# Optimization experiments

Measured on AMD Instinct MI355X. Metric: run time of the kernel, lower is better.

## Reference

```python
import jax, jax.numpy as jnp
import numpy as np

N_NODES = 100_000
N_EDGES = 800_000
N_GRAPHS = 2048
D = 64
NUM_REL = 5
PROP_STEPS = 6
S2S_STEPS = 6


def setup_inputs() -> dict:
    key = jax.random.key(0)
    ks = jax.random.split(key, 16)
    x = jax.random.normal(ks[0], (N_NODES, 15), jnp.float32)
    edge_index = jax.random.randint(ks[1], (2, N_EDGES), 0, N_NODES)
    edge_type = jax.random.randint(ks[2], (N_EDGES,), 0, NUM_REL)
    batch = jnp.sort(jax.random.randint(ks[3], (N_NODES,), 0, N_GRAPHS))

    def lin(k, i, o):
        return jax.random.normal(k, (i, o), jnp.float32) / np.sqrt(i).astype(np.float32)

    return {
        'x': x, 'edge_index': edge_index, 'edge_type': edge_type, 'batch': batch,
        'lin0_w': lin(ks[4], 15, D), 'lin0_b': jnp.zeros((D,), jnp.float32),
        'basis': jax.random.normal(ks[5], (NUM_REL, D, D), jnp.float32) / np.sqrt(D).astype(np.float32),
        'att': jax.random.normal(ks[6], (NUM_REL, NUM_REL), jnp.float32) / np.sqrt(NUM_REL).astype(np.float32),
        'root': lin(ks[7], D, D), 'conv_b': jnp.zeros((D,), jnp.float32),
        'w_ih': jax.random.normal(ks[8], (4 * D, 2 * D), jnp.float32) / np.sqrt(2 * D).astype(np.float32),
        'w_hh': jax.random.normal(ks[9], (4 * D, D), jnp.float32) / np.sqrt(D).astype(np.float32),
        'b_ih': jnp.zeros((4 * D,), jnp.float32), 'b_hh': jnp.zeros((4 * D,), jnp.float32),
        'lin1_w': lin(ks[10], 2 * D, D), 'lin1_b': jnp.zeros((D,), jnp.float32),
        'lin2_w': lin(ks[11], D, 12), 'lin2_b': jnp.zeros((12,), jnp.float32),
    }


def _rgcn_conv(h, src, dst, edge_type, W, root, bias):
    # W: [R, D, D]; transform all nodes per relation, then gather per edge.
    n = h.shape[0]
    h_rel = jnp.einsum('nd,rde->rne', h, W)            # [R, N, D]
    msg = h_rel[edge_type, src]                        # [E, D] gather
    agg = jnp.zeros_like(h).at[dst].add(msg)           # scatter-add
    cnt = jnp.zeros((n,), h.dtype).at[dst].add(1.0)
    agg = agg / jnp.maximum(cnt, 1.0)[:, None]         # mean aggregation
    return agg + h @ root + bias


def _set2set(h, batch, w_ih, w_hh, b_ih, b_hh):
    d = h.shape[1]
    q_star = jnp.zeros((N_GRAPHS, 2 * d), h.dtype)
    hx = jnp.zeros((N_GRAPHS, d), h.dtype)
    cx = jnp.zeros((N_GRAPHS, d), h.dtype)
    for _ in range(S2S_STEPS):
        gates = q_star @ w_ih.T + b_ih + hx @ w_hh.T + b_hh
        i, f, g, o = jnp.split(gates, 4, axis=-1)
        cx = jax.nn.sigmoid(f) * cx + jax.nn.sigmoid(i) * jnp.tanh(g)
        hx = jax.nn.sigmoid(o) * jnp.tanh(cx)
        q = hx                                          # [B, D]
        e = jnp.sum(h * q[batch], axis=-1)              # [N]
        m = jax.ops.segment_max(e, batch, num_segments=N_GRAPHS)
        a = jnp.exp(e - m[batch])
        s = jax.ops.segment_sum(a, batch, num_segments=N_GRAPHS)
        a = a / s[batch]                                # segment softmax
        r = jax.ops.segment_sum(a[:, None] * h, batch, num_segments=N_GRAPHS)
        q_star = jnp.concatenate([q, r], axis=-1)
    return q_star


def reference(x, edge_index, edge_type, batch, lin0_w, lin0_b, basis, att, root,
              conv_b, w_ih, w_hh, b_ih, b_hh, lin1_w, lin1_b, lin2_w, lin2_b):
    W = jnp.einsum('rb,bde->rde', att, basis)           # basis decomposition
    h = jax.nn.relu(x @ lin0_w + lin0_b)
    src, dst = edge_index[0], edge_index[1]
    for _ in range(PROP_STEPS):
        h = jax.nn.relu(_rgcn_conv(h, src, dst, edge_type, W, root, conv_b))
    q = _set2set(h, batch, w_ih, w_hh, b_ih, b_hh)      # [B, 2D]
    out = jax.nn.relu(q @ lin1_w + lin1_b)
    return out @ lin2_w + lin2_b                        # [B, 12]
```

## Files before the change

### kernel.cpp

```cpp
#include <hip/hip_runtime.h>
#include <hip/hip_bf16.h>
#include <math.h>

#define NN 100000
#define NE 800000
#define NG 2048
#define DD 64
#define NR 5
#define KK 384
#define NB ((NN + 255) / 256)
#define CAP 96

typedef __attribute__((ext_vector_type(8))) short bf16x8;
typedef __attribute__((ext_vector_type(4))) float f32x4;
typedef unsigned short ushort_t;
typedef unsigned int uint_t;

static __device__ __forceinline__ float sigmoidf_(float x) { return 1.0f / (1.0f + expf(-x)); }

static __device__ __forceinline__ ushort_t f2bf(float f) {
    uint_t u = __float_as_uint(f);
    uint_t r = (u + 0x7FFFu + ((u >> 16) & 1u)) >> 16;
    return (ushort_t)r;
}
static __device__ __forceinline__ float bf2f(ushort_t b) {
    return __uint_as_float(((uint_t)b) << 16);
}

__global__ void k_w2(const float* __restrict__ att, const float* __restrict__ basis,
                     const float* __restrict__ root, ushort_t* __restrict__ wt_hi,
                     ushort_t* __restrict__ wt_lo) {
    int i = blockIdx.x * blockDim.x + threadIdx.x;
    if (i >= DD * KK) return;
    int c = i / KK;
    int k = i % KK;
    int t = k >> 6;
    int kd = k & 63;
    float w;
    if (t < NR) {
        w = 0.f;
#pragma unroll
        for (int b = 0; b < NR; ++b) w += att[t * NR + b] * basis[(b * DD + kd) * DD + c];
    } else {
        w = root[kd * DD + c];
    }
    ushort_t hi = f2bf(w);
    ushort_t lo = f2bf(w - bf2f(hi));
    wt_hi[c * KK + k] = hi;
    wt_lo[c * KK + k] = lo;
}

__global__ void k_wf(const float* __restrict__ wih, const float* __restrict__ whh,
                     const float* __restrict__ bih, const float* __restrict__ bhh,
                     float* __restrict__ Wq, float* __restrict__ Wr, float* __restrict__ Wb) {
    int i = blockIdx.x * blockDim.x + threadIdx.x;
    if (i >= 256 * 64) return;
    int j = i >> 6, c = i & 63;
    Wq[i] = wih[j * 128 + c] + whh[i];
    Wr[i] = wih[j * 128 + 64 + c];
    if (c == 0) Wb[j] = bih[j] + bhh[j];
}

__global__ void k_cnt(const int* __restrict__ dst, int* __restrict__ deg) {
    int e = blockIdx.x * blockDim.x + threadIdx.x;
    if (e < NE) atomicAdd(&deg[dst[e]], 1);
}

__global__ void k_scan1(const int* __restrict__ deg, int* __restrict__ part,
                        int* __restrict__ bsum) {
    __shared__ int s[256];
    int tid = threadIdx.x;
    int i = blockIdx.x * 256 + tid;
    int v = (i < NN) ? deg[i] : 0;
    s[tid] = v;
    __syncthreads();
    for (int off = 1; off < 256; off <<= 1) {
        int t = (tid >= off) ? s[tid - off] : 0;
        __syncthreads();
        s[tid] += t;
        __syncthreads();
    }
    if (i < NN) part[i] = s[tid] - v;
    if (tid == 255) bsum[blockIdx.x] = s[255];
}

__global__ void k_scan2(int* __restrict__ bsum) {
    __shared__ int s[512];
    int tid = threadIdx.x;
    int v = (tid < NB) ? bsum[tid] : 0;
    s[tid] = v;
    __syncthreads();
    for (int off = 1; off < 512; off <<= 1) {
        int t = (tid >= off) ? s[tid - off] : 0;
        __syncthreads();
        s[tid] += t;
        __syncthreads();
    }
    if (tid < NB) bsum[tid] = s[tid] - v;
}

__global__ void k_scan3(const int* __restrict__ part, const int* __restrict__ bsum,
                        const int* __restrict__ deg, int* __restrict__ rowptr,
                        float* __restrict__ invc) {
    int i = blockIdx.x * blockDim.x + threadIdx.x;
    if (i >= NN) return;
    rowptr[i] = part[i] + bsum[i >> 8];
    invc[i] = 1.0f / fmaxf((float)deg[i], 1.0f);
    if (i == 0) rowptr[NN] = NE;
}

__global__ void k_fill(const int* __restrict__ src, const int* __restrict__ dst,
                       const int* __restrict__ et, int* __restrict__ cur,
                       int* __restrict__ eidx) {
    int e = blockIdx.x * blockDim.x + threadIdx.x;
    if (e >= NE) return;
    int d = dst[e];
    int pos = atomicAdd(&cur[d], 1);
    eidx[pos] = src[e] | (et[e] << 20);
}

__global__ void k_seg(const int* __restrict__ batch, int* __restrict__ seg) {
    int g = blockIdx.x * blockDim.x + threadIdx.x;
    if (g > NG) return;
    int lo = 0, hi = NN;
    while (lo < hi) {
        int mid = (lo + hi) >> 1;
        if (batch[mid] < g) lo = mid + 1; else hi = mid;
    }
    seg[g] = lo;
}

__global__ void k_lin0(const float* __restrict__ x, const float* __restrict__ w,
                       const float* __restrict__ b, float* __restrict__ h) {
    int lane = threadIdx.x & 63, wave = threadIdx.x >> 6;
    float Wc[15];
#pragma unroll
    for (int k = 0; k < 15; ++k) Wc[k] = w[k * DD + lane];
    float bias = b[lane];
    int n0 = blockIdx.x * 256;
    int n1 = min(n0 + 256, NN);
    for (int n = n0 + wave; n < n1; n += 4) {
        int nu = __builtin_amdgcn_readfirstlane(n);
        const float* xr = x + (size_t)nu * 15;
        float a = bias;
#pragma unroll
        for (int k = 0; k < 15; ++k) a += xr[k] * Wc[k];
        h[(size_t)nu * DD + lane] = fmaxf(a, 0.f);
    }
}

__global__ void __launch_bounds__(512) k_conv(
        const float* __restrict__ h, const int* __restrict__ eidx,
        const int* __restrict__ rowptr, const float* __restrict__ invc,
        const ushort_t* __restrict__ wt_hi, const ushort_t* __restrict__ wt_lo,
        const float* __restrict__ bias, float* __restrict__ hout) {
    __shared__ ushort_t lhi[32][392];
    __shared__ ushort_t llo[32][392];
    int tid = threadIdx.x;
    int lane = tid & 63, w = tid >> 6;
    int n0 = blockIdx.x * 32;

    for (int i = 0; i < 4; ++i) {
        int row = w * 4 + i;
        int n = __builtin_amdgcn_readfirstlane(n0 + row);
        int r0 = rowptr[n], r1 = rowptr[n + 1];
        float a0 = 0.f, a1 = 0.f, a2 = 0.f, a3 = 0.f, a4 = 0.f;
        int e = r0;
        for (; e + 8 <= r1; e += 8) {
            int p0 = eidx[e + 0], p1 = eidx[e + 1], p2 = eidx[e + 2], p3 = eidx[e + 3];
            int p4 = eidx[e + 4], p5 = eidx[e + 5], p6 = eidx[e + 6], p7 = eidx[e + 7];
            float v0 = h[(size_t)(p0 & 0xFFFFF) * DD + lane];
            float v1 = h[(size_t)(p1 & 0xFFFFF) * DD + lane];
            float v2 = h[(size_t)(p2 & 0xFFFFF) * DD + lane];
            float v3 = h[(size_t)(p3 & 0xFFFFF) * DD + lane];
            float v4 = h[(size_t)(p4 & 0xFFFFF) * DD + lane];
            float v5 = h[(size_t)(p5 & 0xFFFFF) * DD + lane];
            float v6 = h[(size_t)(p6 & 0xFFFFF) * DD + lane];
            float v7 = h[(size_t)(p7 & 0xFFFFF) * DD + lane];
            int t0 = p0 >> 20, t1 = p1 >> 20, t2 = p2 >> 20, t3 = p3 >> 20;
            int t4 = p4 >> 20, t5 = p5 >> 20, t6 = p6 >> 20, t7 = p7 >> 20;
            a0 += (t0 == 0 ? v0 : 0.f) + (t1 == 0 ? v1 : 0.f) + (t2 == 0 ? v2 : 0.f) + (t3 == 0 ? v3 : 0.f)
                + (t4 == 0 ? v4 : 0.f) + (t5 == 0 ? v5 : 0.f) + (t6 == 0 ? v6 : 0.f) + (t7 == 0 ? v7 : 0.f);
            a1 += (t0 == 1 ? v0 : 0.f) + (t1 == 1 ? v1 : 0.f) + (t2 == 1 ? v2 : 0.f) + (t3 == 1 ? v3 : 0.f)
                + (t4 == 1 ? v4 : 0.f) + (t5 == 1 ? v5 : 0.f) + (t6 == 1 ? v6 : 0.f) + (t7 == 1 ? v7 : 0.f);
            a2 += (t0 == 2 ? v0 : 0.f) + (t1 == 2 ? v1 : 0.f) + (t2 == 2 ? v2 : 0.f) + (t3 == 2 ? v3 : 0.f)
                + (t4 == 2 ? v4 : 0.f) + (t5 == 2 ? v5 : 0.f) + (t6 == 2 ? v6 : 0.f) + (t7 == 2 ? v7 : 0.f);
            a3 += (t0 == 3 ? v0 : 0.f) + (t1 == 3 ? v1 : 0.f) + (t2 == 3 ? v2 : 0.f) + (t3 == 3 ? v3 : 0.f)
                + (t4 == 3 ? v4 : 0.f) + (t5 == 3 ? v5 : 0.f) + (t6 == 3 ? v6 : 0.f) + (t7 == 3 ? v7 : 0.f);
            a4 += (t0 == 4 ? v0 : 0.f) + (t1 == 4 ? v1 : 0.f) + (t2 == 4 ? v2 : 0.f) + (t3 == 4 ? v3 : 0.f)
                + (t4 == 4 ? v4 : 0.f) + (t5 == 4 ? v5 : 0.f) + (t6 == 4 ? v6 : 0.f) + (t7 == 4 ? v7 : 0.f);
        }
        for (; e + 4 <= r1; e += 4) {
            int p0 = eidx[e + 0], p1 = eidx[e + 1], p2 = eidx[e + 2], p3 = eidx[e + 3];
            float v0 = h[(size_t)(p0 & 0xFFFFF) * DD + lane];
            float v1 = h[(size_t)(p1 & 0xFFFFF) * DD + lane];
            float v2 = h[(size_t)(p2 & 0xFFFFF) * DD + lane];
            float v3 = h[(size_t)(p3 & 0xFFFFF) * DD + lane];
            int t0 = p0 >> 20, t1 = p1 >> 20, t2 = p2 >> 20, t3 = p3 >> 20;
            a0 += (t0 == 0 ? v0 : 0.f) + (t1 == 0 ? v1 : 0.f) + (t2 == 0 ? v2 : 0.f) + (t3 == 0 ? v3 : 0.f);
            a1 += (t0 == 1 ? v0 : 0.f) + (t1 == 1 ? v1 : 0.f) + (t2 == 1 ? v2 : 0.f) + (t3 == 1 ? v3 : 0.f);
            a2 += (t0 == 2 ? v0 : 0.f) + (t1 == 2 ? v1 : 0.f) + (t2 == 2 ? v2 : 0.f) + (t3 == 2 ? v3 : 0.f);
            a3 += (t0 == 3 ? v0 : 0.f) + (t1 == 3 ? v1 : 0.f) + (t2 == 3 ? v2 : 0.f) + (t3 == 3 ? v3 : 0.f);
            a4 += (t0 == 4 ? v0 : 0.f) + (t1 == 4 ? v1 : 0.f) + (t2 == 4 ? v2 : 0.f) + (t3 == 4 ? v3 : 0.f);
        }
        for (; e < r1; ++e) {
            int p = eidx[e];
            float v = h[(size_t)(p & 0xFFFFF) * DD + lane];
            int t = p >> 20;
            a0 += (t == 0) ? v : 0.f;
            a1 += (t == 1) ? v : 0.f;
            a2 += (t == 2) ? v : 0.f;
            a3 += (t == 3) ? v : 0.f;
            a4 += (t == 4) ? v : 0.f;
        }
        float ic = invc[n];
        float vals[6];
        vals[0] = a0 * ic; vals[1] = a1 * ic; vals[2] = a2 * ic;
        vals[3] = a3 * ic; vals[4] = a4 * ic;
        vals[5] = h[(size_t)n * DD + lane];
#pragma unroll
        for (int t = 0; t < 6; ++t) {
            ushort_t hi = f2bf(vals[t]);
            ushort_t lo = f2bf(vals[t] - bf2f(hi));
            lhi[row][t * 64 + lane] = hi;
            llo[row][t * 64 + lane] = lo;
        }
    }
    __syncthreads();

    int rg = w & 1;
    int ct = w >> 1;
    int crow = lane & 15, kb = lane >> 4;
    const ushort_t* pbh = wt_hi + (size_t)(ct * 16 + crow) * KK + kb * 8;
    const ushort_t* pbl = wt_lo + (size_t)(ct * 16 + crow) * KK + kb * 8;
    f32x4 acc = (f32x4){0.f, 0.f, 0.f, 0.f};
#pragma unroll 3
    for (int ks = 0; ks < 12; ++ks) {
        bf16x8 ahi = *(const bf16x8*)&lhi[rg * 16 + crow][ks * 32 + kb * 8];
        bf16x8 alo = *(const bf16x8*)&llo[rg * 16 + crow][ks * 32 + kb * 8];
        bf16x8 bhi = *(const bf16x8*)(pbh + ks * 32);
        bf16x8 blo = *(const bf16x8*)(pbl + ks * 32);
        acc = __builtin_amdgcn_mfma_f32_16x16x32_bf16(ahi, bhi, acc, 0, 0, 0);
        acc = __builtin_amdgcn_mfma_f32_16x16x32_bf16(ahi, blo, acc, 0, 0, 0);
        acc = __builtin_amdgcn_mfma_f32_16x16x32_bf16(alo, bhi, acc, 0, 0, 0);
    }
    float bv = bias[ct * 16 + crow];
#pragma unroll
    for (int r = 0; r < 4; ++r) {
        int n = n0 + rg * 16 + kb * 4 + r;
        hout[(size_t)n * DD + ct * 16 + crow] = fmaxf(acc[r] + bv, 0.f);
    }
}

__global__ void __launch_bounds__(256) k_s2s6(
        const float* __restrict__ h, const int* __restrict__ seg,
        const float* __restrict__ Wq, const float* __restrict__ Wr,
        const float* __restrict__ Wb, float* __restrict__ qstar) {
    int g = blockIdx.x;
    int tid = threadIdx.x;
    int lane = tid & 63, wave = tid >> 6;
    __shared__ float hsm[CAP][65];
    __shared__ float a_s[256];
    __shared__ float gates_s[256];
    __shared__ float hx_s[64], cx_s[64], r_s[64];
    __shared__ float red_s[4][64];
    __shared__ float m_s, sum_s;

    int s0 = seg[g], s1 = seg[g + 1];
    int len = min(s1 - s0, 256);
    int cap = min(len, CAP);
    for (int i = tid; i < cap * 64; i += 256) {
        int row = i >> 6, c = i & 63;
        hsm[row][c] = h[(size_t)(s0 + row) * DD + c];
    }
    if (tid < 64) { hx_s[tid] = 0.f; cx_s[tid] = 0.f; r_s[tid] = 0.f; }
    __syncthreads();

    for (int step = 0; step < 6; ++step) {
        {
            float acc = Wb[tid];
            const float4* wq4 = (const float4*)(Wq + (size_t)tid * DD);
            const float4* wr4 = (const float4*)(Wr + (size_t)tid * DD);
            const float4* hx4 = (const float4*)hx_s;
            const float4* rr4 = (const float4*)r_s;
#pragma unroll 4
            for (int k4 = 0; k4 < 16; ++k4) {
                float4 wv = wq4[k4], hv = hx4[k4];
                acc += wv.x * hv.x + wv.y * hv.y + wv.z * hv.z + wv.w * hv.w;
            }
#pragma unroll 4
            for (int k4 = 0; k4 < 16; ++k4) {
                float4 wv = wr4[k4], rv = rr4[k4];
                acc += wv.x * rv.x + wv.y * rv.y + wv.z * rv.z + wv.w * rv.w;
            }
            gates_s[tid] = acc;
        }
        __syncthreads();
        if (tid < 64) {
            float iv = sigmoidf_(gates_s[tid]);
            float fv = sigmoidf_(gates_s[64 + tid]);
            float gv = tanhf(gates_s[128 + tid]);
            float ov = sigmoidf_(gates_s[192 + tid]);
            float cc = fv * cx_s[tid] + iv * gv;
            cx_s[tid] = cc;
            hx_s[tid] = ov * tanhf(cc);
        }
        __syncthreads();

        for (int row = tid; row < len; row += 256) {
            const float* hr = (row < CAP) ? &hsm[row][0] : &h[(size_t)(s0 + row) * DD];
            float e = 0.f;
#pragma unroll 8
            for (int c = 0; c < 64; ++c) e += hr[c] * hx_s[c];
            a_s[row] = e;
        }
        __syncthreads();
        if (wave == 0) {
            float mm = -INFINITY;
            for (int row = lane; row < len; row += 64) mm = fmaxf(mm, a_s[row]);
#pragma unroll
            for (int off = 32; off >= 1; off >>= 1) mm = fmaxf(mm, __shfl_xor(mm, off, 64));
            if (lane == 0) m_s = mm;
        }
        __syncthreads();
        float m = m_s;
        for (int row = tid; row < len; row += 256) a_s[row] = expf(a_s[row] - m);
        __syncthreads();
        if (wave == 0) {
            float ss = 0.f;
            for (int row = lane; row < len; row += 64) ss += a_s[row];
#pragma unroll
            for (int off = 32; off >= 1; off >>= 1) ss += __shfl_xor(ss, off, 64);
            if (lane == 0) sum_s = ss;
        }
        __syncthreads();
        float racc = 0.f;
        for (int row = wave; row < len; row += 4) {
            const float* hr = (row < CAP) ? &hsm[row][0] : &h[(size_t)(s0 + row) * DD];
            racc += a_s[row] * hr[lane];
        }
        red_s[wave][lane] = racc;
        __syncthreads();
        if (tid < 64) {
            float r = red_s[0][tid] + red_s[1][tid] + red_s[2][tid] + red_s[3][tid];
            float s = sum_s;
            r_s[tid] = (s > 0.f) ? (r / s) : 0.f;
        }
        __syncthreads();
    }
    if (tid < 64) {
        qstar[(size_t)g * 2 * DD + tid] = hx_s[tid];
        qstar[(size_t)g * 2 * DD + DD + tid] = r_s[tid];
    }
}

__global__ void k_final(const float* __restrict__ qstar, const float* __restrict__ w1,
                        const float* __restrict__ b1, const float* __restrict__ w2,
                        const float* __restrict__ b2, float* __restrict__ out) {
    int g = blockIdx.x;
    int j = threadIdx.x;
    float a = b1[j];
    const float* qs = qstar + (size_t)g * 2 * DD;
#pragma unroll 16
    for (int k = 0; k < 2 * DD; ++k) a += qs[k] * w1[k * DD + j];
    float t = fmaxf(a, 0.f);
    __shared__ float ts[64];
    ts[j] = t;
    __syncthreads();
    if (j < 12) {
        float o = b2[j];
#pragma unroll 16
        for (int d = 0; d < DD; ++d) o += ts[d] * w2[d * 12 + j];
        out[(size_t)g * 12 + j] = o;
    }
}

extern "C" void kernel_launch(void* const* d_in, const int* in_sizes, int n_in,
                              void* d_out, int out_size, void* d_ws, size_t ws_size,
                              hipStream_t stream) {
    const float* x     = (const float*)d_in[0];
    const int*   ei    = (const int*)d_in[1];
    const int*   etype = (const int*)d_in[2];
    const int*   batch = (const int*)d_in[3];
    const float* l0w   = (const float*)d_in[4];
    const float* l0b   = (const float*)d_in[5];
    const float* basis = (const float*)d_in[6];
    const float* att   = (const float*)d_in[7];
    const float* root  = (const float*)d_in[8];
    const float* convb = (const float*)d_in[9];
    const float* wih   = (const float*)d_in[10];
    const float* whh   = (const float*)d_in[11];
    const float* bih   = (const float*)d_in[12];
    const float* bhh   = (const float*)d_in[13];
    const float* l1w   = (const float*)d_in[14];
    const float* l1b   = (const float*)d_in[15];
    const float* l2w   = (const float*)d_in[16];
    const float* l2b   = (const float*)d_in[17];
    const int* src = ei;
    const int* dst = ei + NE;
    float* out = (float*)d_out;

    char* ws = (char*)d_ws;
    size_t off = 0;
    auto alloc = [&](size_t bytes) {
        void* p = ws + off;
        off = (off + bytes + 255) & ~(size_t)255;
        return p;
    };
    ushort_t* wt_hi = (ushort_t*)alloc((size_t)DD * KK * 2);
    ushort_t* wt_lo = (ushort_t*)alloc((size_t)DD * KK * 2);
    float* Wq     = (float*)alloc((size_t)256 * 64 * 4);
    float* Wr     = (float*)alloc((size_t)256 * 64 * 4);
    float* Wb     = (float*)alloc((size_t)256 * 4);
    float* h_a    = (float*)alloc((size_t)NN * DD * 4);
    float* h_b    = (float*)alloc((size_t)NN * DD * 4);
    int*   deg    = (int*)alloc((size_t)NN * 4);
    float* invc   = (float*)alloc((size_t)NN * 4);
    int*   part   = (int*)alloc((size_t)NN * 4);
    int*   bsum   = (int*)alloc((size_t)512 * 4);
    int*   rowptr = (int*)alloc((size_t)(NN + 1) * 4);
    int*   cur    = (int*)alloc((size_t)NN * 4);
    int*   eidx   = (int*)alloc((size_t)NE * 4);
    int*   seg    = (int*)alloc((size_t)(NG + 1) * 4);
    float* qstar  = (float*)alloc((size_t)NG * 2 * DD * 4);

    hipMemsetAsync(deg, 0, (size_t)NN * 4, stream);

    k_cnt<<<(NE + 255) / 256, 256, 0, stream>>>(dst, deg);
    k_scan1<<<NB, 256, 0, stream>>>(deg, part, bsum);
    k_scan2<<<1, 512, 0, stream>>>(bsum);
    k_scan3<<<(NN + 255) / 256, 256, 0, stream>>>(part, bsum, deg, rowptr, invc);
    hipMemcpyAsync(cur, rowptr, (size_t)NN * 4, hipMemcpyDeviceToDevice, stream);
    k_fill<<<(NE + 255) / 256, 256, 0, stream>>>(src, dst, etype, cur, eidx);

    k_w2<<<(DD * KK + 255) / 256, 256, 0, stream>>>(att, basis, root, wt_hi, wt_lo);
    k_wf<<<(256 * 64 + 255) / 256, 256, 0, stream>>>(wih, whh, bih, bhh, Wq, Wr, Wb);
    k_seg<<<(NG + 256) / 256, 256, 0, stream>>>(batch, seg);
    k_lin0<<<(NN + 255) / 256, 256, 0, stream>>>(x, l0w, l0b, h_a);

    for (int s = 0; s < 6; ++s) {
        const float* hin = (s & 1) ? h_b : h_a;
        float* hout      = (s & 1) ? h_a : h_b;
        k_conv<<<NN / 32, 512, 0, stream>>>(hin, eidx, rowptr, invc,
                                            wt_hi, wt_lo, convb, hout);
    }

    k_s2s6<<<NG, 256, 0, stream>>>(h_a, seg, Wq, Wr, Wb, qstar);

    k_final<<<NG, 64, 0, stream>>>(qstar, l1w, l1b, l2w, l2b, out);
}
```

Before: 1.020 ms.

## Gather conv edges block-wide with LDS atomics; transpose set2set gate weights

The RGCN conv kernel no longer has each wave walk the edge lists of its own 4 nodes. All 8 waves now stride over the block's whole 32-node edge range and accumulate per-(node, relation) sums into shared memory with atomics. To allow this, the destination node's low 5 bits are packed into each edge index. The aim is to balance gather work across waves regardless of node degree, at the cost of LDS atomic contention, an extra zero-fill and barrier, and fewer independent loads in flight per wave than the old 8-way unrolled loop. Separately, the set2set LSTM gate weights are stored transposed so that threads read consecutive addresses when computing gates.

```diff
diff --git a/kernel.cpp b/kernel.cpp
--- a/kernel.cpp
+++ b/kernel.cpp
@@ -52,12 +52,12 @@
 
 __global__ void k_wf(const float* __restrict__ wih, const float* __restrict__ whh,
                      const float* __restrict__ bih, const float* __restrict__ bhh,
-                     float* __restrict__ Wq, float* __restrict__ Wr, float* __restrict__ Wb) {
+                     float* __restrict__ WqT, float* __restrict__ WrT, float* __restrict__ Wb) {
     int i = blockIdx.x * blockDim.x + threadIdx.x;
-    if (i >= 256 * 64) return;
-    int j = i >> 6, c = i & 63;
-    Wq[i] = wih[j * 128 + c] + whh[i];
-    Wr[i] = wih[j * 128 + 64 + c];
+    if (i >= 64 * 256) return;
+    int c = i >> 8, j = i & 255;
+    WqT[i] = wih[j * 128 + c] + whh[j * 64 + c];
+    WrT[i] = wih[j * 128 + 64 + c];
     if (c == 0) Wb[j] = bih[j] + bhh[j];
 }
 
@@ -116,7 +116,7 @@
     if (e >= NE) return;
     int d = dst[e];
     int pos = atomicAdd(&cur[d], 1);
-    eidx[pos] = src[e] | (et[e] << 20);
+    eidx[pos] = src[e] | (et[e] << 20) | ((d & 31) << 23);
 }
 
 __global__ void k_seg(const int* __restrict__ batch, int* __restrict__ seg) {
@@ -154,74 +154,45 @@
         const int* __restrict__ rowptr, const float* __restrict__ invc,
         const ushort_t* __restrict__ wt_hi, const ushort_t* __restrict__ wt_lo,
         const float* __restrict__ bias, float* __restrict__ hout) {
-    __shared__ ushort_t lhi[32][392];
-    __shared__ ushort_t llo[32][392];
+    __shared__ __align__(16) char smem[50176];
+    float (*accf)[NR][64] = reinterpret_cast<float (*)[NR][64]>(smem);
+    ushort_t (*lhi)[392] = reinterpret_cast<ushort_t (*)[392]>(smem);
+    ushort_t (*llo)[392] = reinterpret_cast<ushort_t (*)[392]>(smem + 25088);
+
     int tid = threadIdx.x;
     int lane = tid & 63, w = tid >> 6;
     int n0 = blockIdx.x * 32;
 
+    for (int i = tid; i < 32 * NR * 64; i += 512) ((float*)smem)[i] = 0.f;
+    __syncthreads();
+
+    int e0 = rowptr[n0], e1 = rowptr[n0 + 32];
+    for (int e = e0 + w; e < e1; e += 8) {
+        int p = eidx[e];
+        float v = h[(size_t)(p & 0xFFFFF) * DD + lane];
+        atomicAdd(&accf[(p >> 23) & 31][(p >> 20) & 7][lane], v);
+    }
+    __syncthreads();
+
+    float myv[4][6];
+#pragma unroll
     for (int i = 0; i < 4; ++i) {
         int row = w * 4 + i;
-        int n = __builtin_amdgcn_readfirstlane(n0 + row);
-        int r0 = rowptr[n], r1 = rowptr[n + 1];
-        float a0 = 0.f, a1 = 0.f, a2 = 0.f, a3 = 0.f, a4 = 0.f;
-        int e = r0;
-        for (; e + 8 <= r1; e += 8) {
-            int p0 = eidx[e + 0], p1 = eidx[e + 1], p2 = eidx[e + 2], p3 = eidx[e + 3];
-            int p4 = eidx[e + 4], p5 = eidx[e + 5], p6 = eidx[e + 6], p7 = eidx[e + 7];
-            float v0 = h[(size_t)(p0 & 0xFFFFF) * DD + lane];
-            float v1 = h[(size_t)(p1 & 0xFFFFF) * DD + lane];
-            float v2 = h[(size_t)(p2 & 0xFFFFF) * DD + lane];
-            float v3 = h[(size_t)(p3 & 0xFFFFF) * DD + lane];
-            float v4 = h[(size_t)(p4 & 0xFFFFF) * DD + lane];
-            float v5 = h[(size_t)(p5 & 0xFFFFF) * DD + lane];
-            float v6 = h[(size_t)(p6 & 0xFFFFF) * DD + lane];
-            float v7 = h[(size_t)(p7 & 0xFFFFF) * DD + lane];
-            int t0 = p0 >> 20, t1 = p1 >> 20, t2 = p2 >> 20, t3 = p3 >> 20;
-            int t4 = p4 >> 20, t5 = p5 >> 20, t6 = p6 >> 20, t7 = p7 >> 20;
-            a0 += (t0 == 0 ? v0 : 0.f) + (t1 == 0 ? v1 : 0.f) + (t2 == 0 ? v2 : 0.f) + (t3 == 0 ? v3 : 0.f)
-                + (t4 == 0 ? v4 : 0.f) + (t5 == 0 ? v5 : 0.f) + (t6 == 0 ? v6 : 0.f) + (t7 == 0 ? v7 : 0.f);
-            a1 += (t0 == 1 ? v0 : 0.f) + (t1 == 1 ? v1 : 0.f) + (t2 == 1 ? v2 : 0.f) + (t3 == 1 ? v3 : 0.f)
-                + (t4 == 1 ? v4 : 0.f) + (t5 == 1 ? v5 : 0.f) + (t6 == 1 ? v6 : 0.f) + (t7 == 1 ? v7 : 0.f);
-            a2 += (t0 == 2 ? v0 : 0.f) + (t1 == 2 ? v1 : 0.f) + (t2 == 2 ? v2 : 0.f) + (t3 == 2 ? v3 : 0.f)
-                + (t4 == 2 ? v4 : 0.f) + (t5 == 2 ? v5 : 0.f) + (t6 == 2 ? v6 : 0.f) + (t7 == 2 ? v7 : 0.f);
-            a3 += (t0 == 3 ? v0 : 0.f) + (t1 == 3 ? v1 : 0.f) + (t2 == 3 ? v2 : 0.f) + (t3 == 3 ? v3 : 0.f)
-                + (t4 == 3 ? v4 : 0.f) + (t5 == 3 ? v5 : 0.f) + (t6 == 3 ? v6 : 0.f) + (t7 == 3 ? v7 : 0.f);
-            a4 += (t0 == 4 ? v0 : 0.f) + (t1 == 4 ? v1 : 0.f) + (t2 == 4 ? v2 : 0.f) + (t3 == 4 ? v3 : 0.f)
-                + (t4 == 4 ? v4 : 0.f) + (t5 == 4 ? v5 : 0.f) + (t6 == 4 ? v6 : 0.f) + (t7 == 4 ? v7 : 0.f);
-        }
-        for (; e + 4 <= r1; e += 4) {
-            int p0 = eidx[e + 0], p1 = eidx[e + 1], p2 = eidx[e + 2], p3 = eidx[e + 3];
-            float v0 = h[(size_t)(p0 & 0xFFFFF) * DD + lane];
-            float v1 = h[(size_t)(p1 & 0xFFFFF) * DD + lane];
-            float v2 = h[(size_t)(p2 & 0xFFFFF) * DD + lane];
-            float v3 = h[(size_t)(p3 & 0xFFFFF) * DD + lane];
-            int t0 = p0 >> 20, t1 = p1 >> 20, t2 = p2 >> 20, t3 = p3 >> 20;
-            a0 += (t0 == 0 ? v0 : 0.f) + (t1 == 0 ? v1 : 0.f) + (t2 == 0 ? v2 : 0.f) + (t3 == 0 ? v3 : 0.f);
-            a1 += (t0 == 1 ? v0 : 0.f) + (t1 == 1 ? v1 : 0.f) + (t2 == 1 ? v2 : 0.f) + (t3 == 1 ? v3 : 0.f);
-            a2 += (t0 == 2 ? v0 : 0.f) + (t1 == 2 ? v1 : 0.f) + (t2 == 2 ? v2 : 0.f) + (t3 == 2 ? v3 : 0.f);
-            a3 += (t0 == 3 ? v0 : 0.f) + (t1 == 3 ? v1 : 0.f) + (t2 == 3 ? v2 : 0.f) + (t3 == 3 ? v3 : 0.f);
-            a4 += (t0 == 4 ? v0 : 0.f) + (t1 == 4 ? v1 : 0.f) + (t2 == 4 ? v2 : 0.f) + (t3 == 4 ? v3 : 0.f);
-        }
-        for (; e < r1; ++e) {
-            int p = eidx[e];
-            float v = h[(size_t)(p & 0xFFFFF) * DD + lane];
-            int t = p >> 20;
-            a0 += (t == 0) ? v : 0.f;
-            a1 += (t == 1) ? v : 0.f;
-            a2 += (t == 2) ? v : 0.f;
-            a3 += (t == 3) ? v : 0.f;
-            a4 += (t == 4) ? v : 0.f;
-        }
+        int n = n0 + row;
         float ic = invc[n];
-        float vals[6];
-        vals[0] = a0 * ic; vals[1] = a1 * ic; vals[2] = a2 * ic;
-        vals[3] = a3 * ic; vals[4] = a4 * ic;
-        vals[5] = h[(size_t)n * DD + lane];
+#pragma unroll
+        for (int t = 0; t < NR; ++t) myv[i][t] = accf[row][t][lane] * ic;
+        myv[i][5] = h[(size_t)n * DD + lane];
+    }
+    __syncthreads();
+
+#pragma unroll
+    for (int i = 0; i < 4; ++i) {
+        int row = w * 4 + i;
 #pragma unroll
         for (int t = 0; t < 6; ++t) {
-            ushort_t hi = f2bf(vals[t]);
-            ushort_t lo = f2bf(vals[t] - bf2f(hi));
+            ushort_t hi = f2bf(myv[i][t]);
+            ushort_t lo = f2bf(myv[i][t] - bf2f(hi));
             lhi[row][t * 64 + lane] = hi;
             llo[row][t * 64 + lane] = lo;
         }
@@ -254,7 +225,7 @@
 
 __global__ void __launch_bounds__(256) k_s2s6(
         const float* __restrict__ h, const int* __restrict__ seg,
-        const float* __restrict__ Wq, const float* __restrict__ Wr,
+        const float* __restrict__ WqT, const float* __restrict__ WrT,
         const float* __restrict__ Wb, float* __restrict__ qstar) {
     int g = blockIdx.x;
     int tid = threadIdx.x;
@@ -279,20 +250,9 @@
     for (int step = 0; step < 6; ++step) {
         {
             float acc = Wb[tid];
-            const float4* wq4 = (const float4*)(Wq + (size_t)tid * DD);
-            const float4* wr4 = (const float4*)(Wr + (size_t)tid * DD);
-            const float4* hx4 = (const float4*)hx_s;
-            const float4* rr4 = (const float4*)r_s;
-#pragma unroll 4
-            for (int k4 = 0; k4 < 16; ++k4) {
-                float4 wv = wq4[k4], hv = hx4[k4];
-                acc += wv.x * hv.x + wv.y * hv.y + wv.z * hv.z + wv.w * hv.w;
-            }
-#pragma unroll 4
-            for (int k4 = 0; k4 < 16; ++k4) {
-                float4 wv = wr4[k4], rv = rr4[k4];
-                acc += wv.x * rv.x + wv.y * rv.y + wv.z * rv.z + wv.w * rv.w;
-            }
+#pragma unroll 8
+            for (int c = 0; c < 64; ++c)
+                acc += hx_s[c] * WqT[c * 256 + tid] + r_s[c] * WrT[c * 256 + tid];
             gates_s[tid] = acc;
         }
         __syncthreads();
@@ -409,8 +369,8 @@
     };
     ushort_t* wt_hi = (ushort_t*)alloc((size_t)DD * KK * 2);
     ushort_t* wt_lo = (ushort_t*)alloc((size_t)DD * KK * 2);
-    float* Wq     = (float*)alloc((size_t)256 * 64 * 4);
-    float* Wr     = (float*)alloc((size_t)256 * 64 * 4);
+    float* WqT    = (float*)alloc((size_t)64 * 256 * 4);
+    float* WrT    = (float*)alloc((size_t)64 * 256 * 4);
     float* Wb     = (float*)alloc((size_t)256 * 4);
     float* h_a    = (float*)alloc((size_t)NN * DD * 4);
     float* h_b    = (float*)alloc((size_t)NN * DD * 4);
@@ -434,7 +394,7 @@
     k_fill<<<(NE + 255) / 256, 256, 0, stream>>>(src, dst, etype, cur, eidx);
 
     k_w2<<<(DD * KK + 255) / 256, 256, 0, stream>>>(att, basis, root, wt_hi, wt_lo);
-    k_wf<<<(256 * 64 + 255) / 256, 256, 0, stream>>>(wih, whh, bih, bhh, Wq, Wr, Wb);
+    k_wf<<<(64 * 256 + 255) / 256, 256, 0, stream>>>(wih, whh, bih, bhh, WqT, WrT, Wb);
     k_seg<<<(NG + 256) / 256, 256, 0, stream>>>(batch, seg);
     k_lin0<<<(NN + 255) / 256, 256, 0, stream>>>(x, l0w, l0b, h_a);
 
@@ -445,7 +405,7 @@
                                             wt_hi, wt_lo, convb, hout);
     }
 
-    k_s2s6<<<NG, 256, 0, stream>>>(h_a, seg, Wq, Wr, Wb, qstar);
+    k_s2s6<<<NG, 256, 0, stream>>>(h_a, seg, WqT, WrT, Wb, qstar);
 
     k_final<<<NG, 64, 0, stream>>>(qstar, l1w, l1b, l2w, l2b, out);
 }
```

Measured after the change: 2.190 ms. 115% more time.
